# Optimization experiments

Measured on AMD Instinct MI355X. Metric: run time of the kernel, lower is better.

The kernel has to match this reference:

```python
import jax, jax.numpy as jnp
import numpy as np

IN_DIM = 128
OUT_DIM = 128
BATCH = 1024
K = 3        # spline order
INIT_G = 3   # initial number of grid intervals


def setup_inputs() -> dict:
    key = jax.random.key(0)
    k1, k2 = jax.random.split(key)
    x = jax.random.normal(k1, (BATCH, IN_DIM), dtype=jnp.float32)
    # grid as in __init__: arange(-k, G+k+1)*h + (-1), tiled per (in,out) edge
    h = (1.0 - (-1.0)) / INIT_G
    grid_row = jnp.arange(-K, INIT_G + K + 1, dtype=jnp.float32) * h - 1.0  # (G+2k+1,) = (10,)
    grid = jnp.tile(grid_row[None, :], (IN_DIM * OUT_DIM, 1))               # (E, 10)
    n_basis = grid.shape[1] - 1 - K                                          # 6
    c_basis = 0.1 * jax.random.normal(k2, (IN_DIM * OUT_DIM, n_basis), dtype=jnp.float32)
    c_spl = jnp.ones(IN_DIM * OUT_DIM, dtype=jnp.float32)
    c_res = jnp.ones(IN_DIM * OUT_DIM, dtype=jnp.float32)
    return {"x": x, "grid": grid, "c_basis": c_basis, "c_spl": c_spl, "c_res": c_res}


def get_spline_basis(x_ext, grid, k=K):
    # x_ext: (E, B), grid: (E, G)
    g = grid[:, :, None]      # (E, G, 1)
    x = x_ext[:, None, :]     # (E, 1, B)
    b = ((x >= g[:, :-1]) & (x < g[:, 1:])).astype(x_ext.dtype)  # (E, G-1, B)
    for KK in range(1, k + 1):  # Cox-de Boor recursion; k is a small static constant
        left = (x - g[:, :-(KK + 1)]) / (g[:, KK:-1] - g[:, :-(KK + 1)])
        right = (g[:, KK + 1:] - x) / (g[:, KK + 1:] - g[:, 1:-KK])
        b = left * b[:, :-1] + right * b[:, 1:]
    return b  # (E, G-1-k, B)


def reference(x, grid, c_basis, c_spl, c_res):
    batch, in_dim = x.shape
    out_dim = c_spl.shape[0] // in_dim
    # broadcast each input feature to every output: edge index = o*in_dim + i
    x_ext = jnp.broadcast_to(x[:, None, :], (batch, out_dim, in_dim)).reshape(batch, in_dim * out_dim).T  # (E, B)
    res = jax.nn.swish(x_ext).T                                  # (B, E) residual activation
    Bi = get_spline_basis(x_ext, grid, K)                        # (E, 6, B)
    spl = jnp.einsum('ej,ejb->eb', c_basis, Bi).T                # (B, E)
    y = c_spl[None, :] * spl + c_res[None, :] * res              # (B, E)
    y = y.reshape(batch, out_dim, in_dim).sum(axis=2) / in_dim   # (B, out_dim)
    grid_r = grid.reshape(out_dim, in_dim, -1)
    input_norm = grid_r[:, :, -1] - grid_r[:, :, 0] + 1e-05      # (out, in)
    spl_reg = jnp.mean(jnp.abs(spl.reshape(batch, out_dim, in_dim)), axis=0) / input_norm
    return (y, spl_reg)
```

## Files before the change

### kernel.cpp

```cpp
#include <hip/hip_runtime.h>

static constexpr int BATCH   = 1024;
static constexpr int IN_DIM  = 128;
static constexpr int OUT_DIM = 128;
static constexpr int NEDGE   = IN_DIM * OUT_DIM;
static constexpr int Y_SIZE  = BATCH * OUT_DIM;

static constexpr size_t P_OFF  = 0;
static constexpr size_t P2_OFF = (size_t)NEDGE * 4;

__device__ __forceinline__ void eval_basis(
    float xv, const float* tg, const float* inv1, const float* inv2,
    const float* inv3, float* bb )
{
#pragma unroll
    for (int m = 0; m < 9; ++m)
        bb[m] = (xv >= tg[m] && xv < tg[m + 1]) ? 1.0f : 0.0f;
#pragma unroll
    for (int m = 0; m < 8; ++m)
        bb[m] = (xv - tg[m]) * inv1[m] * bb[m]
              + (tg[m + 2] - xv) * inv1[m + 1] * bb[m + 1];
#pragma unroll
    for (int m = 0; m < 7; ++m)
        bb[m] = (xv - tg[m]) * inv2[m] * bb[m]
              + (tg[m + 3] - xv) * inv2[m + 1] * bb[m + 1];
#pragma unroll
    for (int m = 0; m < 6; ++m)
        bb[m] = (xv - tg[m]) * inv3[m] * bb[m]
              + (tg[m + 4] - xv) * inv3[m + 1] * bb[m + 1];
}

__global__ __launch_bounds__(256) void k_fused(
    const float* __restrict__ x, const float* __restrict__ grid,
    const float* __restrict__ c_basis, const float* __restrict__ c_spl,
    const float* __restrict__ c_res, float* __restrict__ ws)
{
    __shared__ float4 smem4[2048];
    const int t   = threadIdx.x;
    const int blk = blockIdx.x;

    float tg[10];
#pragma unroll
    for (int m = 0; m < 10; ++m) tg[m] = grid[m];
    float inv1[9], inv2[8], inv3[7];
#pragma unroll
    for (int m = 0; m < 9; ++m) inv1[m] = 1.0f / (tg[m + 1] - tg[m]);
#pragma unroll
    for (int m = 0; m < 8; ++m) inv2[m] = 1.0f / (tg[m + 2] - tg[m]);
#pragma unroll
    for (int m = 0; m < 7; ++m) inv3[m] = 1.0f / (tg[m + 3] - tg[m]);

    if (blk < 512) {
        const int bt = blk >> 5;
        const int ot = (blk >> 4) & 1;
        const int ic = blk & 15;
        const int b0 = bt * 64, o0 = ot * 64, i0 = ic * 8;
        float4* Fl = smem4;
        float4* Wl = smem4 + 1024;

        const int bl  = t & 63;
        const int iig = t >> 6;
        const int oo  = t >> 2;
#pragma unroll
        for (int k = 0; k < 2; ++k) {
            const int   ii = iig * 2 + k;
            const float xv = x[(size_t)(b0 + bl) * IN_DIM + i0 + ii];
            float bb[9];
            eval_basis(xv, tg, inv1, inv2, inv3, bb);
            const float sw = xv / (1.0f + expf(-xv));
            const int xr = (bl >> 2) & 1;
            Fl[ii * 128 + ((bl * 2)     ^ xr)] = make_float4(bb[0], bb[1], bb[2], bb[3]);
            Fl[ii * 128 + ((bl * 2 + 1) ^ xr)] = make_float4(bb[4], bb[5], sw, 0.f);

            const int iw = (t & 3) * 2 + k;
            const int e  = (o0 + oo) * IN_DIM + i0 + iw;
            const float cs = c_spl[e];
            const float cr = c_res[e];
            const float* cb = c_basis + (size_t)e * 6;
            const int xw = ((oo >> 2) & 3) << 1;
            Wl[oo * 16 + ((iw * 2)     ^ xw)] =
                make_float4(cs * cb[0], cs * cb[1], cs * cb[2], cs * cb[3]);
            Wl[oo * 16 + ((iw * 2 + 1) ^ xw)] =
                make_float4(cs * cb[4], cs * cb[5], cr, 0.f);
        }
        __syncthreads();

        const int bi  = t & 15;
        const int og4 = t >> 4;
        float acc[4][4];
#pragma unroll
        for (int c = 0; c < 4; ++c)
#pragma unroll
            for (int q = 0; q < 4; ++q) acc[c][q] = 0.f;

#pragma unroll 2
        for (int ii = 0; ii < 8; ++ii) {
            float4 fb[4][2], wo[4][2];
#pragma unroll
            for (int c = 0; c < 4; ++c) {
                const int b  = bi + 16 * c;
                const int xr = (b >> 2) & 1;
                fb[c][0] = Fl[ii * 128 + ((b * 2)     ^ xr)];
                fb[c][1] = Fl[ii * 128 + ((b * 2 + 1) ^ xr)];
            }
#pragma unroll
            for (int q = 0; q < 4; ++q) {
                const int o  = og4 * 4 + q;
                const int xr = (og4 & 3) << 1;
                wo[q][0] = Wl[o * 16 + ((ii * 2)     ^ xr)];
                wo[q][1] = Wl[o * 16 + ((ii * 2 + 1) ^ xr)];
            }
#pragma unroll
            for (int c = 0; c < 4; ++c)
#pragma unroll
                for (int q = 0; q < 4; ++q) {
                    acc[c][q] += fb[c][0].x * wo[q][0].x + fb[c][0].y * wo[q][0].y
                               + fb[c][0].z * wo[q][0].z + fb[c][0].w * wo[q][0].w
                               + fb[c][1].x * wo[q][1].x + fb[c][1].y * wo[q][1].y
                               + fb[c][1].z * wo[q][1].z + fb[c][1].w * wo[q][1].w;
                }
        }

        float4* P2 = reinterpret_cast<float4*>(ws + P2_OFF);
#pragma unroll
        for (int c = 0; c < 4; ++c)
            P2[((size_t)ic * Y_SIZE
                + (size_t)(b0 + bi + 16 * c) * OUT_DIM + o0 + og4 * 4) >> 2] =
                make_float4(acc[c][0], acc[c][1], acc[c][2], acc[c][3]);
    } else {
        float4* Bl  = smem4;
        float4* CBl = smem4 + 512;
        float*  partial = reinterpret_cast<float*>(smem4 + 768);
        const int rb = blk - 512;
        const int i  = rb >> 2;
        const int bq = rb & 3;

        const float xv = x[(size_t)(bq * 256 + t) * IN_DIM + i];
        float bb[9];
        eval_basis(xv, tg, inv1, inv2, inv3, bb);
        {
            const int idx = ((t & 31) * 8 + (t >> 5)) * 2;
            Bl[idx]     = make_float4(bb[0], bb[1], bb[2], bb[3]);
            Bl[idx + 1] = make_float4(bb[4], bb[5], 0.f, 0.f);
        }
        if (t < 128) {
            const float* cbp = c_basis + (size_t)(t * IN_DIM + i) * 6;
            CBl[t * 2]     = make_float4(cbp[0], cbp[1], cbp[2], cbp[3]);
            CBl[t * 2 + 1] = make_float4(cbp[4], cbp[5], 0.f, 0.f);
        }
        __syncthreads();

        const int og = t >> 3;
        const int sl = t & 7;
        float4 w0[4], w1[4];
#pragma unroll
        for (int q = 0; q < 4; ++q) {
            w0[q] = CBl[(og * 4 + q) * 2];
            w1[q] = CBl[(og * 4 + q) * 2 + 1];
        }
        float acc[4] = {0.f, 0.f, 0.f, 0.f};
#pragma unroll 4
        for (int bl = 0; bl < 32; ++bl) {
            const float4 f0 = Bl[(bl * 8 + sl) * 2];
            const float4 f1 = Bl[(bl * 8 + sl) * 2 + 1];
#pragma unroll
            for (int q = 0; q < 4; ++q) {
                const float spl = f0.x * w0[q].x + f0.y * w0[q].y
                                + f0.z * w0[q].z + f0.w * w0[q].w
                                + f1.x * w1[q].x + f1.y * w1[q].y;
                acc[q] += fabsf(spl);
            }
        }
#pragma unroll
        for (int q = 0; q < 4; ++q)
            partial[(og * 4 + q) * 9 + sl] = acc[q];
        __syncthreads();
        if (t < 128) {
            float s = 0.f;
#pragma unroll
            for (int k = 0; k < 8; ++k) s += partial[t * 9 + k];
            ws[P_OFF + ((size_t)(t * IN_DIM + i) << 2) + bq] = s;
        }
    }
}

__global__ __launch_bounds__(256) void k_final(
    const float* __restrict__ ws, const float* __restrict__ grid,
    float* __restrict__ out)
{
    const int t   = threadIdx.x;
    const int blk = blockIdx.x;
    if (blk < 128) {
        const int gid = blk * 256 + t;
        const float4* P2 = reinterpret_cast<const float4*>(ws + P2_OFF);
        float4 s = P2[gid];
#pragma unroll
        for (int ic = 1; ic < 16; ++ic) {
            const float4 p = P2[(size_t)ic * (Y_SIZE / 4) + gid];
            s.x += p.x; s.y += p.y; s.z += p.z; s.w += p.w;
        }
        const float sc = 1.0f / (float)IN_DIM;
        reinterpret_cast<float4*>(out)[gid] =
            make_float4(s.x * sc, s.y * sc, s.z * sc, s.w * sc);
    } else {
        const int e = (blk - 128) * 256 + t;
        const float4 p = reinterpret_cast<const float4*>(ws + P_OFF)[e];
        const float invfac = 1.0f / ((float)BATCH * (grid[9] - grid[0] + 1e-5f));
        out[Y_SIZE + e] = (p.x + p.y + p.z + p.w) * invfac;
    }
}

extern "C" void kernel_launch(void* const* d_in, const int* in_sizes, int n_in,
                              void* d_out, int out_size, void* d_ws, size_t ws_size,
                              hipStream_t stream)
{
    const float* x  = (const float*)d_in[0];
    const float* gr = (const float*)d_in[1];
    const float* cb = (const float*)d_in[2];
    const float* cs = (const float*)d_in[3];
    const float* cr = (const float*)d_in[4];
    float* out = (float*)d_out;
    float* ws  = (float*)d_ws;

    k_fused<<<1024, 256, 0, stream>>>(x, gr, cb, cs, cr, ws);
    k_final<<<192, 256, 0, stream>>>(ws, gr, out);
}
```

Before: 80.09 us.

## Fuse spline regularizer accumulation into main contraction blocks, drop separate reg blocks

The spline-regularizer computation, which previously ran in 512 separate blocks that re-evaluated the B-spline basis, now happens inside the main contraction loop. Each thread accumulates |spl| per (o, i) alongside the output sum, and c_spl/c_res are applied after the dot product instead of being pre-folded into the weights. Per-block partials are reduced with wave shuffles and written to a new workspace region, which the final kernel sums across 16 batch tiles. This halves the grid and removes redundant basis evaluation, at the cost of 32 extra accumulator registers, the shuffle reductions and a larger partial buffer.

```diff
diff --git a/kernel.cpp b/kernel.cpp
--- a/kernel.cpp
+++ b/kernel.cpp
@@ -6,8 +6,8 @@
 static constexpr int NEDGE   = IN_DIM * OUT_DIM;
 static constexpr int Y_SIZE  = BATCH * OUT_DIM;
 
-static constexpr size_t P_OFF  = 0;
-static constexpr size_t P2_OFF = (size_t)NEDGE * 4;
+static constexpr size_t P2_OFF = 0;
+static constexpr size_t PS_OFF = (size_t)16 * BATCH * OUT_DIM;
 
 __device__ __forceinline__ void eval_basis(
     float xv, const float* tg, const float* inv1, const float* inv2,
@@ -50,138 +50,101 @@
 #pragma unroll
     for (int m = 0; m < 7; ++m) inv3[m] = 1.0f / (tg[m + 3] - tg[m]);
 
-    if (blk < 512) {
-        const int bt = blk >> 5;
-        const int ot = (blk >> 4) & 1;
-        const int ic = blk & 15;
-        const int b0 = bt * 64, o0 = ot * 64, i0 = ic * 8;
-        float4* Fl = smem4;
-        float4* Wl = smem4 + 1024;
+    const int bt = blk >> 5;
+    const int ot = (blk >> 4) & 1;
+    const int ic = blk & 15;
+    const int b0 = bt * 64, o0 = ot * 64, i0 = ic * 8;
+    float4* Fl = smem4;
+    float4* Wl = smem4 + 1024;
 
-        const int bl  = t & 63;
-        const int iig = t >> 6;
-        const int oo  = t >> 2;
+    const int bl  = t & 63;
+    const int oo  = t >> 2;
 #pragma unroll
-        for (int k = 0; k < 2; ++k) {
-            const int   ii = iig * 2 + k;
-            const float xv = x[(size_t)(b0 + bl) * IN_DIM + i0 + ii];
-            float bb[9];
-            eval_basis(xv, tg, inv1, inv2, inv3, bb);
-            const float sw = xv / (1.0f + expf(-xv));
-            const int xr = (bl >> 2) & 1;
-            Fl[ii * 128 + ((bl * 2)     ^ xr)] = make_float4(bb[0], bb[1], bb[2], bb[3]);
-            Fl[ii * 128 + ((bl * 2 + 1) ^ xr)] = make_float4(bb[4], bb[5], sw, 0.f);
+    for (int k = 0; k < 2; ++k) {
+        const int   ii = (t >> 6) * 2 + k;
+        const float xv = x[(size_t)(b0 + bl) * IN_DIM + i0 + ii];
+        float bb[9];
+        eval_basis(xv, tg, inv1, inv2, inv3, bb);
+        const float sw = xv / (1.0f + expf(-xv));
+        const int xr = (bl >> 2) & 1;
+        Fl[ii * 128 + ((bl * 2)     ^ xr)] = make_float4(bb[0], bb[1], bb[2], bb[3]);
+        Fl[ii * 128 + ((bl * 2 + 1) ^ xr)] = make_float4(bb[4], bb[5], sw, 0.f);
 
-            const int iw = (t & 3) * 2 + k;
-            const int e  = (o0 + oo) * IN_DIM + i0 + iw;
-            const float cs = c_spl[e];
-            const float cr = c_res[e];
-            const float* cb = c_basis + (size_t)e * 6;
-            const int xw = ((oo >> 2) & 3) << 1;
-            Wl[oo * 16 + ((iw * 2)     ^ xw)] =
-                make_float4(cs * cb[0], cs * cb[1], cs * cb[2], cs * cb[3]);
-            Wl[oo * 16 + ((iw * 2 + 1) ^ xw)] =
-                make_float4(cs * cb[4], cs * cb[5], cr, 0.f);
+        const int iw = (t & 3) * 2 + k;
+        const int e  = (o0 + oo) * IN_DIM + i0 + iw;
+        const float cs = c_spl[e];
+        const float cr = c_res[e];
+        const float* cb = c_basis + (size_t)e * 6;
+        const int xw = ((oo >> 2) & 3) << 1;
+        Wl[oo * 16 + ((iw * 2)     ^ xw)] = make_float4(cb[0], cb[1], cb[2], cb[3]);
+        Wl[oo * 16 + ((iw * 2 + 1) ^ xw)] = make_float4(cb[4], cb[5], cs, cr);
+    }
+    __syncthreads();
+
+    const int bi  = t & 15;
+    const int og4 = t >> 4;
+    float acc[4][4];
+    float sacc[4][8];
+#pragma unroll
+    for (int c = 0; c < 4; ++c)
+#pragma unroll
+        for (int q = 0; q < 4; ++q) acc[c][q] = 0.f;
+#pragma unroll
+    for (int q = 0; q < 4; ++q)
+#pragma unroll
+        for (int ii = 0; ii < 8; ++ii) sacc[q][ii] = 0.f;
+
+#pragma unroll
+    for (int ii = 0; ii < 8; ++ii) {
+        float4 fb[4][2], wo[4][2];
+#pragma unroll
+        for (int c = 0; c < 4; ++c) {
+            const int b  = bi + 16 * c;
+            const int xr = (b >> 2) & 1;
+            fb[c][0] = Fl[ii * 128 + ((b * 2)     ^ xr)];
+            fb[c][1] = Fl[ii * 128 + ((b * 2 + 1) ^ xr)];
         }
-        __syncthreads();
-
-        const int bi  = t & 15;
-        const int og4 = t >> 4;
-        float acc[4][4];
+#pragma unroll
+        for (int q = 0; q < 4; ++q) {
+            const int o  = og4 * 4 + q;
+            const int xr = (og4 & 3) << 1;
+            wo[q][0] = Wl[o * 16 + ((ii * 2)     ^ xr)];
+            wo[q][1] = Wl[o * 16 + ((ii * 2 + 1) ^ xr)];
+        }
 #pragma unroll
         for (int c = 0; c < 4; ++c)
 #pragma unroll
-            for (int q = 0; q < 4; ++q) acc[c][q] = 0.f;
+            for (int q = 0; q < 4; ++q) {
+                const float spl =
+                      fb[c][0].x * wo[q][0].x + fb[c][0].y * wo[q][0].y
+                    + fb[c][0].z * wo[q][0].z + fb[c][0].w * wo[q][0].w
+                    + fb[c][1].x * wo[q][1].x + fb[c][1].y * wo[q][1].y;
+                acc[c][q] += wo[q][1].z * spl
+                           + wo[q][1].w * fb[c][1].z;
+                sacc[q][ii] += fabsf(spl);
+            }
+    }
 
-#pragma unroll 2
+    float4* P2 = reinterpret_cast<float4*>(ws + P2_OFF);
+#pragma unroll
+    for (int c = 0; c < 4; ++c)
+        P2[((size_t)ic * Y_SIZE
+            + (size_t)(b0 + bi + 16 * c) * OUT_DIM + o0 + og4 * 4) >> 2] =
+            make_float4(acc[c][0], acc[c][1], acc[c][2], acc[c][3]);
+
+#pragma unroll
+    for (int q = 0; q < 4; ++q)
+#pragma unroll
         for (int ii = 0; ii < 8; ++ii) {
-            float4 fb[4][2], wo[4][2];
-#pragma unroll
-            for (int c = 0; c < 4; ++c) {
-                const int b  = bi + 16 * c;
-                const int xr = (b >> 2) & 1;
-                fb[c][0] = Fl[ii * 128 + ((b * 2)     ^ xr)];
-                fb[c][1] = Fl[ii * 128 + ((b * 2 + 1) ^ xr)];
-            }
-#pragma unroll
-            for (int q = 0; q < 4; ++q) {
-                const int o  = og4 * 4 + q;
-                const int xr = (og4 & 3) << 1;
-                wo[q][0] = Wl[o * 16 + ((ii * 2)     ^ xr)];
-                wo[q][1] = Wl[o * 16 + ((ii * 2 + 1) ^ xr)];
-            }
-#pragma unroll
-            for (int c = 0; c < 4; ++c)
-#pragma unroll
-                for (int q = 0; q < 4; ++q) {
-                    acc[c][q] += fb[c][0].x * wo[q][0].x + fb[c][0].y * wo[q][0].y
-                               + fb[c][0].z * wo[q][0].z + fb[c][0].w * wo[q][0].w
-                               + fb[c][1].x * wo[q][1].x + fb[c][1].y * wo[q][1].y
-                               + fb[c][1].z * wo[q][1].z + fb[c][1].w * wo[q][1].w;
-                }
+            float v = sacc[q][ii];
+            v += __shfl_xor(v, 1);
+            v += __shfl_xor(v, 2);
+            v += __shfl_xor(v, 4);
+            v += __shfl_xor(v, 8);
+            if (bi == 0)
+                ws[PS_OFF + (((size_t)ic * OUT_DIM + o0 + og4 * 4 + q) * 8 + ii)
+                              * 16 + bt] = v;
         }
-
-        float4* P2 = reinterpret_cast<float4*>(ws + P2_OFF);
-#pragma unroll
-        for (int c = 0; c < 4; ++c)
-            P2[((size_t)ic * Y_SIZE
-                + (size_t)(b0 + bi + 16 * c) * OUT_DIM + o0 + og4 * 4) >> 2] =
-                make_float4(acc[c][0], acc[c][1], acc[c][2], acc[c][3]);
-    } else {
-        float4* Bl  = smem4;
-        float4* CBl = smem4 + 512;
-        float*  partial = reinterpret_cast<float*>(smem4 + 768);
-        const int rb = blk - 512;
-        const int i  = rb >> 2;
-        const int bq = rb & 3;
-
-        const float xv = x[(size_t)(bq * 256 + t) * IN_DIM + i];
-        float bb[9];
-        eval_basis(xv, tg, inv1, inv2, inv3, bb);
-        {
-            const int idx = ((t & 31) * 8 + (t >> 5)) * 2;
-            Bl[idx]     = make_float4(bb[0], bb[1], bb[2], bb[3]);
-            Bl[idx + 1] = make_float4(bb[4], bb[5], 0.f, 0.f);
-        }
-        if (t < 128) {
-            const float* cbp = c_basis + (size_t)(t * IN_DIM + i) * 6;
-            CBl[t * 2]     = make_float4(cbp[0], cbp[1], cbp[2], cbp[3]);
-            CBl[t * 2 + 1] = make_float4(cbp[4], cbp[5], 0.f, 0.f);
-        }
-        __syncthreads();
-
-        const int og = t >> 3;
-        const int sl = t & 7;
-        float4 w0[4], w1[4];
-#pragma unroll
-        for (int q = 0; q < 4; ++q) {
-            w0[q] = CBl[(og * 4 + q) * 2];
-            w1[q] = CBl[(og * 4 + q) * 2 + 1];
-        }
-        float acc[4] = {0.f, 0.f, 0.f, 0.f};
-#pragma unroll 4
-        for (int bl = 0; bl < 32; ++bl) {
-            const float4 f0 = Bl[(bl * 8 + sl) * 2];
-            const float4 f1 = Bl[(bl * 8 + sl) * 2 + 1];
-#pragma unroll
-            for (int q = 0; q < 4; ++q) {
-                const float spl = f0.x * w0[q].x + f0.y * w0[q].y
-                                + f0.z * w0[q].z + f0.w * w0[q].w
-                                + f1.x * w1[q].x + f1.y * w1[q].y;
-                acc[q] += fabsf(spl);
-            }
-        }
-#pragma unroll
-        for (int q = 0; q < 4; ++q)
-            partial[(og * 4 + q) * 9 + sl] = acc[q];
-        __syncthreads();
-        if (t < 128) {
-            float s = 0.f;
-#pragma unroll
-            for (int k = 0; k < 8; ++k) s += partial[t * 9 + k];
-            ws[P_OFF + ((size_t)(t * IN_DIM + i) << 2) + bq] = s;
-        }
-    }
 }
 
 __global__ __launch_bounds__(256) void k_final(
@@ -203,10 +166,18 @@
         reinterpret_cast<float4*>(out)[gid] =
             make_float4(s.x * sc, s.y * sc, s.z * sc, s.w * sc);
     } else {
-        const int e = (blk - 128) * 256 + t;
-        const float4 p = reinterpret_cast<const float4*>(ws + P_OFF)[e];
+        const int idx = (blk - 128) * 256 + t;
+        const int o  = idx >> 7;
+        const int i  = idx & 127;
+        const int ic = i >> 3;
+        const int ii = i & 7;
+        const float4* PS4 = reinterpret_cast<const float4*>(ws + PS_OFF)
+                          + (((size_t)ic * OUT_DIM + o) * 8 + ii) * 4;
+        const float4 a = PS4[0], b = PS4[1], c = PS4[2], d = PS4[3];
         const float invfac = 1.0f / ((float)BATCH * (grid[9] - grid[0] + 1e-5f));
-        out[Y_SIZE + e] = (p.x + p.y + p.z + p.w) * invfac;
+        out[Y_SIZE + idx] =
+            (a.x + a.y + a.z + a.w + b.x + b.y + b.z + b.w
+           + c.x + c.y + c.z + c.w + d.x + d.y + d.z + d.w) * invfac;
     }
 }
 
@@ -222,6 +193,6 @@
     float* out = (float*)d_out;
     float* ws  = (float*)d_ws;
 
-    k_fused<<<1024, 256, 0, stream>>>(x, gr, cb, cs, cr, ws);
+    k_fused<<<512, 256, 0, stream>>>(x, gr, cb, cs, cr, ws);
     k_final<<<192, 256, 0, stream>>>(ws, gr, out);
 }
```

Result: slower. 88.28 us (+10.2%).

## Restructure spl_reg reduction to one output per thread with broadcast basis reads

Applied to the files above, without the earlier changes.

In the regularization blocks, each thread now owns one output feature and half the batch rows, reading basis values from shared memory as wave-uniform broadcasts instead of a 4-outputs-by-8-slices tiling. This removes the 8-way partial reduction and the swizzled store layout. The change also adds a minimum-occupancy hint of 4 to the launch bounds and raises the unroll of the main GEMM-like loop. The trade-off is fewer weights reused per shared-memory load, and possible register spills under the tighter occupancy hint.

```diff
diff --git a/kernel.cpp b/kernel.cpp
--- a/kernel.cpp
+++ b/kernel.cpp
@@ -30,7 +30,7 @@
               + (tg[m + 4] - xv) * inv3[m + 1] * bb[m + 1];
 }
 
-__global__ __launch_bounds__(256) void k_fused(
+__global__ __launch_bounds__(256, 4) void k_fused(
     const float* __restrict__ x, const float* __restrict__ grid,
     const float* __restrict__ c_basis, const float* __restrict__ c_spl,
     const float* __restrict__ c_res, float* __restrict__ ws)
@@ -59,11 +59,10 @@
         float4* Wl = smem4 + 1024;
 
         const int bl  = t & 63;
-        const int iig = t >> 6;
         const int oo  = t >> 2;
 #pragma unroll
         for (int k = 0; k < 2; ++k) {
-            const int   ii = iig * 2 + k;
+            const int   ii = (t >> 6) * 2 + k;
             const float xv = x[(size_t)(b0 + bl) * IN_DIM + i0 + ii];
             float bb[9];
             eval_basis(xv, tg, inv1, inv2, inv3, bb);
@@ -93,7 +92,7 @@
 #pragma unroll
             for (int q = 0; q < 4; ++q) acc[c][q] = 0.f;
 
-#pragma unroll 2
+#pragma unroll 4
         for (int ii = 0; ii < 8; ++ii) {
             float4 fb[4][2], wo[4][2];
 #pragma unroll
@@ -138,11 +137,8 @@
         const float xv = x[(size_t)(bq * 256 + t) * IN_DIM + i];
         float bb[9];
         eval_basis(xv, tg, inv1, inv2, inv3, bb);
-        {
-            const int idx = ((t & 31) * 8 + (t >> 5)) * 2;
-            Bl[idx]     = make_float4(bb[0], bb[1], bb[2], bb[3]);
-            Bl[idx + 1] = make_float4(bb[4], bb[5], 0.f, 0.f);
-        }
+        Bl[t * 2]     = make_float4(bb[0], bb[1], bb[2], bb[3]);
+        Bl[t * 2 + 1] = make_float4(bb[4], bb[5], 0.f, 0.f);
         if (t < 128) {
             const float* cbp = c_basis + (size_t)(t * IN_DIM + i) * 6;
             CBl[t * 2]     = make_float4(cbp[0], cbp[1], cbp[2], cbp[3]);
@@ -150,37 +146,28 @@
         }
         __syncthreads();
 
-        const int og = t >> 3;
-        const int sl = t & 7;
-        float4 w0[4], w1[4];
-#pragma unroll
-        for (int q = 0; q < 4; ++q) {
-            w0[q] = CBl[(og * 4 + q) * 2];
-            w1[q] = CBl[(og * 4 + q) * 2 + 1];
-        }
-        float acc[4] = {0.f, 0.f, 0.f, 0.f};
+        const int o  = t & 127;
+        const int bh = t >> 7;
+        const float4 w0 = CBl[o * 2];
+        const float4 w1 = CBl[o * 2 + 1];
+        const float4* fl = Bl + (size_t)bh * 256;
+        float a0 = 0.f, a1 = 0.f;
 #pragma unroll 4
-        for (int bl = 0; bl < 32; ++bl) {
-            const float4 f0 = Bl[(bl * 8 + sl) * 2];
-            const float4 f1 = Bl[(bl * 8 + sl) * 2 + 1];
-#pragma unroll
-            for (int q = 0; q < 4; ++q) {
-                const float spl = f0.x * w0[q].x + f0.y * w0[q].y
-                                + f0.z * w0[q].z + f0.w * w0[q].w
-                                + f1.x * w1[q].x + f1.y * w1[q].y;
-                acc[q] += fabsf(spl);
-            }
-        }
-#pragma unroll
-        for (int q = 0; q < 4; ++q)
-            partial[(og * 4 + q) * 9 + sl] = acc[q];
+        for (int r = 0; r < 128; r += 2) {
+            const float4 f0 = fl[r * 2 + 0];
+            const float4 f1 = fl[r * 2 + 1];
+            const float4 g0 = fl[r * 2 + 2];
+            const float4 g1 = fl[r * 2 + 3];
+            a0 += fabsf(f0.x * w0.x + f0.y * w0.y + f0.z * w0.z + f0.w * w0.w
+                      + f1.x * w1.x + f1.y * w1.y);
+            a1 += fabsf(g0.x * w0.x + g0.y * w0.y + g0.z * w0.z + g0.w * w0.w
+                      + g1.x * w1.x + g1.y * w1.y);
+        }
+        partial[t] = a0 + a1;
         __syncthreads();
-        if (t < 128) {
-            float s = 0.f;
-#pragma unroll
-            for (int k = 0; k < 8; ++k) s += partial[t * 9 + k];
-            ws[P_OFF + ((size_t)(t * IN_DIM + i) << 2) + bq] = s;
-        }
+        if (t < 128)
+            ws[P_OFF + ((size_t)(t * IN_DIM + i) << 2) + bq] =
+                partial[t] + partial[t + 128];
     }
 }
 
```

Measured after the change: 79.83 us. About the same (-0.3%).

## Interleave GEMM and regularizer blocks, remap reg-block LDS layout, tune unroll/occupancy

Applied to the files above, without the earlier changes.

Interleaves the two block families (GEMM-partial and spl_reg) in groups of 8 so both kinds of work are co-scheduled across CUs instead of the reg blocks forming a tail. The reg branch's LDS layout changes so that each wavefront reads a broadcast basis row while lanes hold different output groups, and coefficients are padded to stride 3. It also adds a min-blocks-per-CU launch bound and raises the inner unroll factor. The risks are register spilling under the occupancy hint and new LDS bank conflicts from the stride-3 coefficient reads.

```diff
diff --git a/kernel.cpp b/kernel.cpp
--- a/kernel.cpp
+++ b/kernel.cpp
@@ -30,7 +30,7 @@
               + (tg[m + 4] - xv) * inv3[m + 1] * bb[m + 1];
 }
 
-__global__ __launch_bounds__(256) void k_fused(
+__global__ __launch_bounds__(256, 4) void k_fused(
     const float* __restrict__ x, const float* __restrict__ grid,
     const float* __restrict__ c_basis, const float* __restrict__ c_spl,
     const float* __restrict__ c_res, float* __restrict__ ws)
@@ -38,6 +38,8 @@
     __shared__ float4 smem4[2048];
     const int t   = threadIdx.x;
     const int blk = blockIdx.x;
+    const int fam = (blk >> 3) & 1;
+    const int idx = ((blk >> 4) << 3) | (blk & 7);
 
     float tg[10];
 #pragma unroll
@@ -50,20 +52,19 @@
 #pragma unroll
     for (int m = 0; m < 7; ++m) inv3[m] = 1.0f / (tg[m + 3] - tg[m]);
 
-    if (blk < 512) {
-        const int bt = blk >> 5;
-        const int ot = (blk >> 4) & 1;
-        const int ic = blk & 15;
+    if (fam == 0) {
+        const int bt = idx >> 5;
+        const int ot = (idx >> 4) & 1;
+        const int ic = idx & 15;
         const int b0 = bt * 64, o0 = ot * 64, i0 = ic * 8;
         float4* Fl = smem4;
         float4* Wl = smem4 + 1024;
 
         const int bl  = t & 63;
-        const int iig = t >> 6;
         const int oo  = t >> 2;
 #pragma unroll
         for (int k = 0; k < 2; ++k) {
-            const int   ii = iig * 2 + k;
+            const int   ii = (t >> 6) * 2 + k;
             const float xv = x[(size_t)(b0 + bl) * IN_DIM + i0 + ii];
             float bb[9];
             eval_basis(xv, tg, inv1, inv2, inv3, bb);
@@ -93,7 +94,7 @@
 #pragma unroll
             for (int q = 0; q < 4; ++q) acc[c][q] = 0.f;
 
-#pragma unroll 2
+#pragma unroll 4
         for (int ii = 0; ii < 8; ++ii) {
             float4 fb[4][2], wo[4][2];
 #pragma unroll
@@ -130,39 +131,36 @@
     } else {
         float4* Bl  = smem4;
         float4* CBl = smem4 + 512;
-        float*  partial = reinterpret_cast<float*>(smem4 + 768);
-        const int rb = blk - 512;
-        const int i  = rb >> 2;
-        const int bq = rb & 3;
+        float*  partial = reinterpret_cast<float*>(smem4 + 896);
+        const int i  = idx >> 2;
+        const int bq = idx & 3;
 
         const float xv = x[(size_t)(bq * 256 + t) * IN_DIM + i];
         float bb[9];
         eval_basis(xv, tg, inv1, inv2, inv3, bb);
-        {
-            const int idx = ((t & 31) * 8 + (t >> 5)) * 2;
-            Bl[idx]     = make_float4(bb[0], bb[1], bb[2], bb[3]);
-            Bl[idx + 1] = make_float4(bb[4], bb[5], 0.f, 0.f);
-        }
+        Bl[t * 2]     = make_float4(bb[0], bb[1], bb[2], bb[3]);
+        Bl[t * 2 + 1] = make_float4(bb[4], bb[5], 0.f, 0.f);
         if (t < 128) {
             const float* cbp = c_basis + (size_t)(t * IN_DIM + i) * 6;
-            CBl[t * 2]     = make_float4(cbp[0], cbp[1], cbp[2], cbp[3]);
-            CBl[t * 2 + 1] = make_float4(cbp[4], cbp[5], 0.f, 0.f);
+            CBl[t * 3]     = make_float4(cbp[0], cbp[1], cbp[2], cbp[3]);
+            CBl[t * 3 + 1] = make_float4(cbp[4], cbp[5], 0.f, 0.f);
         }
         __syncthreads();
 
-        const int og = t >> 3;
-        const int sl = t & 7;
+        const int og = t & 31;
+        const int sl = t >> 5;
         float4 w0[4], w1[4];
 #pragma unroll
         for (int q = 0; q < 4; ++q) {
-            w0[q] = CBl[(og * 4 + q) * 2];
-            w1[q] = CBl[(og * 4 + q) * 2 + 1];
+            w0[q] = CBl[(og * 4 + q) * 3];
+            w1[q] = CBl[(og * 4 + q) * 3 + 1];
         }
         float acc[4] = {0.f, 0.f, 0.f, 0.f};
+        const float4* fl = Bl + (size_t)sl * 64;
 #pragma unroll 4
-        for (int bl = 0; bl < 32; ++bl) {
-            const float4 f0 = Bl[(bl * 8 + sl) * 2];
-            const float4 f1 = Bl[(bl * 8 + sl) * 2 + 1];
+        for (int r = 0; r < 32; ++r) {
+            const float4 f0 = fl[r * 2 + 0];
+            const float4 f1 = fl[r * 2 + 1];
 #pragma unroll
             for (int q = 0; q < 4; ++q) {
                 const float spl = f0.x * w0[q].x + f0.y * w0[q].y
```

Result: no change. 79.79 us (-0.4%).
